# Optimization experiments

Measured on AMD Instinct MI355X. Metric: run time of the kernel, lower is better.

## Reference

```python
import jax, jax.numpy as jnp
import numpy as np
from jax import lax

B, C, T = 8, 512, 4096
K = 3
DILATIONS = (1, 3, 5)
EPS_Q = 1e-5
EPS_SNAKE = 1e-9


def quantize_weight(w):
    # BitNet-1.58-style ternary quantization with per-tensor absmean scale,
    # applied with a straight-through estimator.
    s = jnp.mean(jnp.abs(w))
    wq = jnp.clip(jnp.round(w / (s + EPS_Q)), -1.0, 1.0) * s
    return w + lax.stop_gradient(wq - w)


def bitconv1d(x, w, b, dilation, padding):
    # x: [B, C, T], w: [Cout, Cin, K], b: [Cout]
    y = lax.conv_general_dilated(
        x, quantize_weight(w),
        window_strides=(1,),
        padding=[(padding, padding)],
        rhs_dilation=(dilation,),
        dimension_numbers=("NCH", "OIH", "NCH"),
    )
    return y + b[None, :, None]


def snake_beta(x, alpha_p, beta_p):
    # log-scale parametrization: alpha = exp(alpha_p), beta = exp(beta_p)
    a = jnp.exp(alpha_p)[None, :, None]
    b = jnp.exp(beta_p)[None, :, None]
    return x + (1.0 / (b + EPS_SNAKE)) * jnp.sin(a * x) ** 2


def setup_inputs() -> dict:
    key = jax.random.key(0)
    ks = jax.random.split(key, 7)
    return {
        "x": jax.random.normal(ks[0], (B, C, T), dtype=jnp.float32),
        "w1": jax.random.normal(ks[1], (3, C, C, K), dtype=jnp.float32) * 0.05,
        "b1": jax.random.normal(ks[2], (3, C), dtype=jnp.float32) * 0.01,
        "alpha": jax.random.normal(ks[3], (3, C), dtype=jnp.float32) * 0.1,
        "beta": jax.random.normal(ks[4], (3, C), dtype=jnp.float32) * 0.1,
        "w2": jax.random.normal(ks[5], (3, C, C, K), dtype=jnp.float32) * 0.05,
        "b2": jax.random.normal(ks[6], (3, C), dtype=jnp.float32) * 0.01,
    }


def reference(x, w1, b1, alpha, beta, w2, b2):
    for i, d in enumerate(DILATIONS):
        pad1 = d * (K - 1) // 2
        h = bitconv1d(x, w1[i], b1[i], dilation=d, padding=pad1)
        h = snake_beta(h, alpha[i], beta[i])
        h = bitconv1d(h, w2[i], b2[i], dilation=1, padding=(K - 1) // 2)
        x = x + h
    return x
```

## Files before the change

kernel.cpp:

```cpp
#include <hip/hip_runtime.h>
#include <math.h>
#include <stdint.h>


constexpr int B_ = 8, C_ = 512, T_ = 4096, K_ = 3;
constexpr int WELEM = C_ * C_ * K_;

typedef __bf16 bf16x8 __attribute__((ext_vector_type(8)));
typedef float f32x4 __attribute__((ext_vector_type(4)));
typedef unsigned short u16x8 __attribute__((ext_vector_type(8)));
typedef unsigned short u16x4 __attribute__((ext_vector_type(4)));

constexpr size_t OFF_PART = 0;
constexpr size_t OFF_S = 4096;
constexpr size_t OFF_AE = 8192;
constexpr size_t OFF_IB = 16384;
constexpr size_t OFF_WQ1 = 32768;
constexpr size_t OFF_WQ2 = OFF_WQ1 + (size_t)3 * WELEM * 2;
constexpr size_t NBCT = (size_t)B_ * C_ * T_;
constexpr size_t OFF_PHI = OFF_WQ2 + (size_t)3 * WELEM * 2;
constexpr size_t OFF_PLO = OFF_PHI + NBCT * 2;
constexpr size_t OFF_QHI = OFF_PLO + NBCT * 2;
constexpr size_t OFF_QLO = OFF_QHI + NBCT * 2;

__device__ inline unsigned short bf16_rne(float v) {
  unsigned int u = __builtin_bit_cast(unsigned int, v);
  unsigned int r = u + 0x7FFFu + ((u >> 16) & 1u);
  return (unsigned short)(r >> 16);
}

__global__ __launch_bounds__(256)
void absmean_partial(const float* __restrict__ w1, const float* __restrict__ w2,
                     float* __restrict__ part) {
  __shared__ float red[256];
  const int t = blockIdx.y;
  const float* src = (t < 3) ? (w1 + (size_t)t * WELEM) : (w2 + (size_t)(t - 3) * WELEM);
  const int base = blockIdx.x * (256 * 32);
  float v = 0.f;
#pragma unroll
  for (int j = 0; j < 32; ++j) v += fabsf(src[base + j * 256 + threadIdx.x]);
  red[threadIdx.x] = v;
  __syncthreads();
  for (int s = 128; s > 0; s >>= 1) {
    if (threadIdx.x < (unsigned)s) red[threadIdx.x] += red[threadIdx.x + s];
    __syncthreads();
  }
  if (threadIdx.x == 0) part[t * 96 + blockIdx.x] = red[0];
}

__global__ __launch_bounds__(128)
void absmean_final(const float* __restrict__ part, float* __restrict__ svec) {
  __shared__ float red[128];
  const int t = blockIdx.x;
  red[threadIdx.x] = (threadIdx.x < 96) ? part[t * 96 + threadIdx.x] : 0.f;
  __syncthreads();
  for (int s = 64; s > 0; s >>= 1) {
    if (threadIdx.x < (unsigned)s) red[threadIdx.x] += red[threadIdx.x + s];
    __syncthreads();
  }
  if (threadIdx.x == 0) svec[t] = red[0] / (float)WELEM;
}

__global__ __launch_bounds__(256)
void quantize_kernel(const float* __restrict__ src, unsigned short* __restrict__ dst,
                     const float* __restrict__ svec, int sbase) {
  const int idx = blockIdx.x * 256 + threadIdx.x;
  const int j = idx & 7;
  const int lane = (idx >> 3) & 63;
  const int cot = (idx >> 9) & 31;
  const int rest = idx >> 14;
  const int tap = rest % 3;
  const int rest2 = rest / 3;
  const int cc = rest2 & 15;
  const int st = rest2 >> 4;
  const int co = cot * 16 + (lane & 15);
  const int ci = cc * 32 + (lane >> 4) * 8 + j;
  const float s = svec[sbase + st];
  const float w = src[(((size_t)st * C_ + co) * C_ + ci) * K_ + tap];
  float q = rintf(w / (s + 1e-5f));
  q = fminf(1.f, fmaxf(-1.f, q));
  dst[idx] = (unsigned short)(__builtin_bit_cast(unsigned int, q) >> 16);
}

__global__ __launch_bounds__(256)
void snake_params_kernel(const float* __restrict__ al, const float* __restrict__ be,
                         float* __restrict__ ae, float* __restrict__ ib) {
  const int idx = blockIdx.x * 256 + threadIdx.x;
  if (idx < 3 * C_) {
    ae[idx] = expf(al[idx]);
    ib[idx] = 1.f / (expf(be[idx]) + 1e-9f);
  }
}

__global__ __launch_bounds__(256)
void transpose_split(const float* __restrict__ X, unsigned short* __restrict__ Hi,
                     unsigned short* __restrict__ Lo) {
  __shared__ float tile[64][68];
  const int b = blockIdx.z;
  const int c0 = blockIdx.y * 64;
  const int t0 = blockIdx.x * 64;
  const int tid = threadIdx.x;
  {
    const int cl = tid >> 2, tg = tid & 3;
    const float* src = X + ((size_t)b * C_ + c0 + cl) * T_ + t0 + tg * 16;
    float4 v0 = *(const float4*)(src);
    float4 v1 = *(const float4*)(src + 4);
    float4 v2 = *(const float4*)(src + 8);
    float4 v3 = *(const float4*)(src + 12);
    float* d = &tile[cl][tg * 16];
    *(float4*)(d) = v0; *(float4*)(d + 4) = v1;
    *(float4*)(d + 8) = v2; *(float4*)(d + 12) = v3;
  }
  __syncthreads();
  {
    const int tl = tid >> 2, cg = tid & 3;
    u16x8 h0, h1, l0, l1;
#pragma unroll
    for (int j = 0; j < 16; ++j) {
      const float v = tile[cg * 16 + j][tl];
      const unsigned short hb = bf16_rne(v);
      const float hf = __builtin_bit_cast(float, (unsigned int)hb << 16);
      const unsigned short lb = bf16_rne(v - hf);
      if (j < 8) { h0[j] = hb; l0[j] = lb; }
      else       { h1[j - 8] = hb; l1[j - 8] = lb; }
    }
    const size_t off = ((size_t)b * T_ + t0 + tl) * C_ + c0 + cg * 16;
    *(u16x8*)(Hi + off) = h0; *(u16x8*)(Hi + off + 8) = h1;
    *(u16x8*)(Lo + off) = l0; *(u16x8*)(Lo + off + 8) = l1;
  }
}

template <int DIL, bool SNAKE, bool PLANES, bool WF32>
__global__ __launch_bounds__(256, 3)
void conv_mfma(const unsigned short* __restrict__ Xhi,
               const unsigned short* __restrict__ Xlo,
               const unsigned short* __restrict__ Wq,
               const float* __restrict__ svec,
               const float* __restrict__ bias, const float* __restrict__ aexp,
               const float* __restrict__ invb,
               const float* __restrict__ res,
               float* __restrict__ Y,
               unsigned short* __restrict__ Ohi,
               unsigned short* __restrict__ Olo) {
  constexpr int TT = 128;
  constexpr int R = TT + 2 * DIL;
  constexpr int RW = 40;
  __shared__ unsigned short Xs[2][R * RW];

  const int b = blockIdx.z;
  const int co0 = blockIdx.y * 128;
  const int cob = blockIdx.y * 8;
  const int t0 = blockIdx.x * TT;
  const int tid = threadIdx.x;
  const int lane = tid & 63;
  const int wv = tid >> 6;
  const int l15 = lane & 15;
  const int quad = lane >> 4;

  f32x4 acc[8][2] = {};

  const size_t xbase = (size_t)b * T_ * C_;

#pragma unroll 1
  for (int cc = 0; cc < C_ / 32; ++cc) {
    constexpr int XU = R * 8;
#pragma unroll
    for (int it = 0; it < (XU + 255) / 256; ++it) {
      const int u = it * 256 + tid;
      if (u < XU) {
        const int r = u >> 3, sub = u & 7;
        const int pl = sub >> 2, g = sub & 3;
        const int t = t0 - DIL + r;
        u16x8 v = {0, 0, 0, 0, 0, 0, 0, 0};
        if ((unsigned)t < (unsigned)T_)
          v = *(const u16x8*)((pl ? Xlo : Xhi) + xbase + (size_t)t * C_ + cc * 32 + g * 8);
        *(u16x8*)&Xs[pl][r * RW + g * 8] = v;
      }
    }
    __syncthreads();

#pragma unroll 1
    for (int tap = 0; tap < K_; ++tap) {
      const unsigned short* wb =
          Wq + ((((size_t)cc * K_ + tap) * 32 + cob) * 512) + (size_t)lane * 8;
      bf16x8 a[8];
#pragma unroll
      for (int m = 0; m < 8; ++m)
        a[m] = __builtin_bit_cast(bf16x8, *(const u16x8*)(wb + m * 512));
#pragma unroll
      for (int n = 0; n < 2; ++n) {
        const int r = wv * 32 + n * 16 + l15 + tap * DIL;
        const bf16x8 bh = __builtin_bit_cast(bf16x8, *(const u16x8*)&Xs[0][r * RW + quad * 8]);
        const bf16x8 bl = __builtin_bit_cast(bf16x8, *(const u16x8*)&Xs[1][r * RW + quad * 8]);
#pragma unroll
        for (int m = 0; m < 8; ++m) {
          acc[m][n] = __builtin_amdgcn_mfma_f32_16x16x32_bf16(a[m], bh, acc[m][n], 0, 0, 0);
          acc[m][n] = __builtin_amdgcn_mfma_f32_16x16x32_bf16(a[m], bl, acc[m][n], 0, 0, 0);
        }
      }
    }
    __syncthreads();
  }

  const float sw = *svec;
#pragma unroll
  for (int m = 0; m < 8; ++m) {
    const int cb = co0 + m * 16 + quad * 4;
    float bs[4], av[4], ibv[4];
#pragma unroll
    for (int reg = 0; reg < 4; ++reg) {
      bs[reg] = bias[cb + reg];
      if (SNAKE) { av[reg] = aexp[cb + reg]; ibv[reg] = invb[cb + reg]; }
    }
#pragma unroll
    for (int n = 0; n < 2; ++n) {
      const int t = t0 + wv * 32 + n * 16 + l15;
      float vv[4];
#pragma unroll
      for (int reg = 0; reg < 4; ++reg) {
        float v = sw * acc[m][n][reg] + bs[reg];
        if (SNAKE) {
          const float sn = __sinf(av[reg] * v);
          v = v + ibv[reg] * sn * sn;
        } else {
          v = v + res[((size_t)b * C_ + cb + reg) * T_ + t];
        }
        if (WF32) Y[((size_t)b * C_ + cb + reg) * T_ + t] = v;
        vv[reg] = v;
      }
      if (PLANES) {
        u16x4 hq, lq;
#pragma unroll
        for (int reg = 0; reg < 4; ++reg) {
          const unsigned short hb = bf16_rne(vv[reg]);
          const float hf = __builtin_bit_cast(float, (unsigned int)hb << 16);
          hq[reg] = hb;
          lq[reg] = bf16_rne(vv[reg] - hf);
        }
        const size_t poff = ((size_t)b * T_ + t) * C_ + cb;
        *(u16x4*)(Ohi + poff) = hq;
        *(u16x4*)(Olo + poff) = lq;
      }
    }
  }
}

extern "C" void kernel_launch(void* const* d_in, const int* in_sizes, int n_in,
                              void* d_out, int out_size, void* d_ws, size_t ws_size,
                              hipStream_t stream) {
  (void)in_sizes; (void)n_in; (void)out_size; (void)ws_size;
  const float* x = (const float*)d_in[0];
  const float* w1 = (const float*)d_in[1];
  const float* b1 = (const float*)d_in[2];
  const float* al = (const float*)d_in[3];
  const float* be = (const float*)d_in[4];
  const float* w2 = (const float*)d_in[5];
  const float* b2 = (const float*)d_in[6];
  float* out = (float*)d_out;
  char* wsb = (char*)d_ws;

  float* part = (float*)(wsb + OFF_PART);
  float* svec = (float*)(wsb + OFF_S);
  float* ae = (float*)(wsb + OFF_AE);
  float* ib = (float*)(wsb + OFF_IB);
  unsigned short* wq1 = (unsigned short*)(wsb + OFF_WQ1);
  unsigned short* wq2 = (unsigned short*)(wsb + OFF_WQ2);
  unsigned short* Phi = (unsigned short*)(wsb + OFF_PHI);
  unsigned short* Plo = (unsigned short*)(wsb + OFF_PLO);
  unsigned short* Qhi = (unsigned short*)(wsb + OFF_QHI);
  unsigned short* Qlo = (unsigned short*)(wsb + OFF_QLO);

  absmean_partial<<<dim3(96, 6), 256, 0, stream>>>(w1, w2, part);
  absmean_final<<<6, 128, 0, stream>>>(part, svec);
  quantize_kernel<<<(3 * WELEM) / 256, 256, 0, stream>>>(w1, wq1, svec, 0);
  quantize_kernel<<<(3 * WELEM) / 256, 256, 0, stream>>>(w2, wq2, svec, 3);
  snake_params_kernel<<<6, 256, 0, stream>>>(al, be, ae, ib);

  const dim3 tgrid(T_ / 64, C_ / 64, B_);
  const dim3 cgrid(T_ / 128, C_ / 128, B_);

  transpose_split<<<tgrid, 256, 0, stream>>>(x, Phi, Plo);

  conv_mfma<1, true, true, false><<<cgrid, 256, 0, stream>>>(
      Phi, Plo, wq1 + 0 * (size_t)WELEM, svec + 0, b1 + 0, ae + 0, ib + 0,
      nullptr, nullptr, Qhi, Qlo);
  conv_mfma<1, false, true, true><<<cgrid, 256, 0, stream>>>(
      Qhi, Qlo, wq2 + 0 * (size_t)WELEM, svec + 3, b2 + 0, nullptr, nullptr,
      x, out, Phi, Plo);

  conv_mfma<3, true, true, false><<<cgrid, 256, 0, stream>>>(
      Phi, Plo, wq1 + 1 * (size_t)WELEM, svec + 1, b1 + C_, ae + C_, ib + C_,
      nullptr, nullptr, Qhi, Qlo);
  conv_mfma<1, false, true, true><<<cgrid, 256, 0, stream>>>(
      Qhi, Qlo, wq2 + 1 * (size_t)WELEM, svec + 4, b2 + C_, nullptr, nullptr,
      out, out, Phi, Plo);

  conv_mfma<5, true, true, false><<<cgrid, 256, 0, stream>>>(
      Phi, Plo, wq1 + 2 * (size_t)WELEM, svec + 2, b1 + 2 * C_, ae + 2 * C_,
      ib + 2 * C_, nullptr, nullptr, Qhi, Qlo);
  conv_mfma<1, false, false, true><<<cgrid, 256, 0, stream>>>(
      Qhi, Qlo, wq2 + 2 * (size_t)WELEM, svec + 5, b2 + 2 * C_, nullptr, nullptr,
      out, out, nullptr, nullptr);
}
```

Before: 897.7 us.

## Double-buffer LDS input tiles and stage bf16 plane stores through shared memory

The conv MFMA kernel now keeps two LDS buffers: it loads the next channel chunk from global memory into registers while computing on the current chunk, then writes those registers to the other buffer. This removes one barrier per chunk and hides global-load latency behind the MFMAs. The epilogue for the hi/lo bf16 plane outputs is also reworked to go through LDS, so each thread writes full 16-element contiguous runs per time row instead of scattered 4-element stores. This costs double the LDS, more staging registers (which may cut occupancy under launch_bounds 3), and extra barriers in the epilogue.

```diff
diff --git a/kernel.cpp b/kernel.cpp
--- a/kernel.cpp
+++ b/kernel.cpp
@@ -9,7 +9,6 @@
 typedef __bf16 bf16x8 __attribute__((ext_vector_type(8)));
 typedef float f32x4 __attribute__((ext_vector_type(4)));
 typedef unsigned short u16x8 __attribute__((ext_vector_type(8)));
-typedef unsigned short u16x4 __attribute__((ext_vector_type(4)));
 
 constexpr size_t OFF_PART = 0;
 constexpr size_t OFF_S = 4096;
@@ -145,7 +144,9 @@
   constexpr int TT = 128;
   constexpr int R = TT + 2 * DIL;
   constexpr int RW = 40;
-  __shared__ unsigned short Xs[2][R * RW];
+  constexpr int XU = R * 8;
+  constexpr int NIT = (XU + 255) / 256;
+  __shared__ unsigned short Xs[2][2][R * RW];
 
   const int b = blockIdx.z;
   const int co0 = blockIdx.y * 128;
@@ -161,25 +162,44 @@
 
   const size_t xbase = (size_t)b * T_ * C_;
 
-#pragma unroll 1
-  for (int cc = 0; cc < C_ / 32; ++cc) {
-    constexpr int XU = R * 8;
-#pragma unroll
-    for (int it = 0; it < (XU + 255) / 256; ++it) {
+  auto stage_gload = [&](int cc, u16x8* st) {
+#pragma unroll
+    for (int it = 0; it < NIT; ++it) {
+      const int u = it * 256 + tid;
+      u16x8 v = {0, 0, 0, 0, 0, 0, 0, 0};
+      if (u < XU) {
+        const int r = u >> 3, sub = u & 7;
+        const int pl = sub >> 2, g = sub & 3;
+        const int t = t0 - DIL + r;
+        if ((unsigned)t < (unsigned)T_)
+          v = *(const u16x8*)((pl ? Xlo : Xhi) + xbase + (size_t)t * C_ + cc * 32 + g * 8);
+      }
+      st[it] = v;
+    }
+  };
+  auto stage_swrite = [&](int buf, const u16x8* st) {
+#pragma unroll
+    for (int it = 0; it < NIT; ++it) {
       const int u = it * 256 + tid;
       if (u < XU) {
         const int r = u >> 3, sub = u & 7;
         const int pl = sub >> 2, g = sub & 3;
-        const int t = t0 - DIL + r;
-        u16x8 v = {0, 0, 0, 0, 0, 0, 0, 0};
-        if ((unsigned)t < (unsigned)T_)
-          v = *(const u16x8*)((pl ? Xlo : Xhi) + xbase + (size_t)t * C_ + cc * 32 + g * 8);
-        *(u16x8*)&Xs[pl][r * RW + g * 8] = v;
-      }
-    }
-    __syncthreads();
+        *(u16x8*)&Xs[buf][pl][r * RW + g * 8] = st[it];
+      }
+    }
+  };
+
+  u16x8 st[NIT];
+  stage_gload(0, st);
+  stage_swrite(0, st);
+  __syncthreads();
 
 #pragma unroll 1
+  for (int cc = 0; cc < C_ / 32; ++cc) {
+    const int cur = cc & 1;
+    if (cc < C_ / 32 - 1) stage_gload(cc + 1, st);
+
+#pragma unroll
     for (int tap = 0; tap < K_; ++tap) {
       const unsigned short* wb =
           Wq + ((((size_t)cc * K_ + tap) * 32 + cob) * 512) + (size_t)lane * 8;
@@ -190,8 +210,10 @@
 #pragma unroll
       for (int n = 0; n < 2; ++n) {
         const int r = wv * 32 + n * 16 + l15 + tap * DIL;
-        const bf16x8 bh = __builtin_bit_cast(bf16x8, *(const u16x8*)&Xs[0][r * RW + quad * 8]);
-        const bf16x8 bl = __builtin_bit_cast(bf16x8, *(const u16x8*)&Xs[1][r * RW + quad * 8]);
+        const bf16x8 bh =
+            __builtin_bit_cast(bf16x8, *(const u16x8*)&Xs[cur][0][r * RW + quad * 8]);
+        const bf16x8 bl =
+            __builtin_bit_cast(bf16x8, *(const u16x8*)&Xs[cur][1][r * RW + quad * 8]);
 #pragma unroll
         for (int m = 0; m < 8; ++m) {
           acc[m][n] = __builtin_amdgcn_mfma_f32_16x16x32_bf16(a[m], bh, acc[m][n], 0, 0, 0);
@@ -199,47 +221,94 @@
         }
       }
     }
+
+    if (cc < C_ / 32 - 1) stage_swrite(1 - cur, st);
     __syncthreads();
   }
 
   const float sw = *svec;
-#pragma unroll
-  for (int m = 0; m < 8; ++m) {
-    const int cb = co0 + m * 16 + quad * 4;
-    float bs[4], av[4], ibv[4];
-#pragma unroll
-    for (int reg = 0; reg < 4; ++reg) {
-      bs[reg] = bias[cb + reg];
-      if (SNAKE) { av[reg] = aexp[cb + reg]; ibv[reg] = invb[cb + reg]; }
-    }
-#pragma unroll
-    for (int n = 0; n < 2; ++n) {
-      const int t = t0 + wv * 32 + n * 16 + l15;
-      float vv[4];
+
+  if (PLANES) {
+    uint32_t* E = (uint32_t*)&Xs[0][0][0];
+    constexpr int ELD = 33;
+#pragma unroll 1
+    for (int mb = 0; mb < 4; ++mb) {
+      __syncthreads();
+#pragma unroll
+      for (int mm = 0; mm < 2; ++mm) {
+        const int m = mb * 2 + mm;
+        const int cb = co0 + m * 16 + quad * 4;
+        float bs[4], av[4], ibv[4];
+#pragma unroll
+        for (int reg = 0; reg < 4; ++reg) {
+          bs[reg] = bias[cb + reg];
+          if (SNAKE) { av[reg] = aexp[cb + reg]; ibv[reg] = invb[cb + reg]; }
+        }
+#pragma unroll
+        for (int n = 0; n < 2; ++n) {
+          const int tl = wv * 32 + n * 16 + l15;
+          const int t = t0 + tl;
+#pragma unroll
+          for (int reg = 0; reg < 4; ++reg) {
+            float v = sw * acc[m][n][reg] + bs[reg];
+            if (SNAKE) {
+              const float sn = __sinf(av[reg] * v);
+              v = v + ibv[reg] * sn * sn;
+            } else {
+              v = v + res[((size_t)b * C_ + cb + reg) * T_ + t];
+            }
+            if (WF32) Y[((size_t)b * C_ + cb + reg) * T_ + t] = v;
+            const unsigned short hb = bf16_rne(v);
+            const float hf = __builtin_bit_cast(float, (unsigned int)hb << 16);
+            const unsigned short lb = bf16_rne(v - hf);
+            E[tl * ELD + mm * 16 + quad * 4 + reg] =
+                ((unsigned int)hb << 16) | (unsigned int)lb;
+          }
+        }
+      }
+      __syncthreads();
+      {
+        const int row = tid >> 1, half = tid & 1;
+        uint32_t u[16];
+#pragma unroll
+        for (int j = 0; j < 16; ++j) u[j] = E[row * ELD + half * 16 + j];
+        u16x8 hA, hB, lA, lB;
+#pragma unroll
+        for (int j = 0; j < 8; ++j) {
+          hA[j] = (unsigned short)(u[j] >> 16);
+          lA[j] = (unsigned short)(u[j] & 0xFFFFu);
+          hB[j] = (unsigned short)(u[8 + j] >> 16);
+          lB[j] = (unsigned short)(u[8 + j] & 0xFFFFu);
+        }
+        const size_t poff = ((size_t)b * T_ + t0 + row) * C_ + co0 + mb * 32 + half * 16;
+        *(u16x8*)(Ohi + poff) = hA; *(u16x8*)(Ohi + poff + 8) = hB;
+        *(u16x8*)(Olo + poff) = lA; *(u16x8*)(Olo + poff + 8) = lB;
+      }
+    }
+  } else {
+#pragma unroll
+    for (int m = 0; m < 8; ++m) {
+      const int cb = co0 + m * 16 + quad * 4;
+      float bs[4], av[4], ibv[4];
 #pragma unroll
       for (int reg = 0; reg < 4; ++reg) {
-        float v = sw * acc[m][n][reg] + bs[reg];
-        if (SNAKE) {
-          const float sn = __sinf(av[reg] * v);
-          v = v + ibv[reg] * sn * sn;
-        } else {
-          v = v + res[((size_t)b * C_ + cb + reg) * T_ + t];
-        }
-        if (WF32) Y[((size_t)b * C_ + cb + reg) * T_ + t] = v;
-        vv[reg] = v;
-      }
-      if (PLANES) {
-        u16x4 hq, lq;
+        bs[reg] = bias[cb + reg];
+        if (SNAKE) { av[reg] = aexp[cb + reg]; ibv[reg] = invb[cb + reg]; }
+      }
+#pragma unroll
+      for (int n = 0; n < 2; ++n) {
+        const int t = t0 + wv * 32 + n * 16 + l15;
 #pragma unroll
         for (int reg = 0; reg < 4; ++reg) {
-          const unsigned short hb = bf16_rne(vv[reg]);
-          const float hf = __builtin_bit_cast(float, (unsigned int)hb << 16);
-          hq[reg] = hb;
-          lq[reg] = bf16_rne(vv[reg] - hf);
-        }
-        const size_t poff = ((size_t)b * T_ + t) * C_ + cb;
-        *(u16x4*)(Ohi + poff) = hq;
-        *(u16x4*)(Olo + poff) = lq;
+          float v = sw * acc[m][n][reg] + bs[reg];
+          if (SNAKE) {
+            const float sn = __sinf(av[reg] * v);
+            v = v + ibv[reg] * sn * sn;
+          } else {
+            v = v + res[((size_t)b * C_ + cb + reg) * T_ + t];
+          }
+          Y[((size_t)b * C_ + cb + reg) * T_ + t] = v;
+        }
       }
     }
   }
```

New measurement: 3.085 ms. 3.44x slower.
